# Performance work log

Measured on AMD Instinct MI355X. Metric: run time of the kernel, lower is better.

The kernel has to match this reference:

```python
import jax, jax.numpy as jnp
import numpy as np

N_NODES = 100000
N_EDGES = 1600000
D_IN = 64
D_OUT = 64


def setup_inputs() -> dict:
    key = jax.random.key(0)
    k1, k2, k3, k4 = jax.random.split(key, 4)
    x = jax.random.normal(k1, (N_NODES, D_IN), dtype=jnp.float32)
    edge_index = jax.random.randint(k2, (2, N_EDGES), 0, N_NODES, dtype=jnp.int64)
    W = jax.random.normal(k3, (D_OUT, D_IN), dtype=jnp.float32) * (1.0 / np.sqrt(D_IN))
    b = jax.random.normal(k4, (D_OUT,), dtype=jnp.float32) * 0.01
    return {"x": x, "edge_index": edge_index, "W": W, "b": b}


def reference(x, edge_index, W, b):
    num_nodes = x.shape[0]
    row, col = edge_index[0], edge_index[1]
    # degree of each node as a destination (scatter_add of ones over row)
    deg = jax.ops.segment_sum(jnp.ones(row.shape[0], dtype=x.dtype), row,
                              num_segments=num_nodes)
    # deg^-0.5 with inf (deg==0) replaced by 0
    deg_inv_sqrt = jnp.where(deg > 0, jax.lax.rsqrt(jnp.maximum(deg, 1.0)) * jnp.where(deg > 0, 1.0, 0.0), 0.0)
    deg_inv_sqrt = jnp.where(deg > 0, deg ** -0.5, 0.0)
    # gather source features, scale by source norm, scatter-add to destinations
    weighted = x[col] * deg_inv_sqrt[col][:, None]          # [E, D_IN]
    agg = jax.ops.segment_sum(weighted, row, num_segments=num_nodes)  # [N, D_IN]
    agg = agg * deg_inv_sqrt[:, None]
    # linear + relu (torch Linear: y = agg @ W.T + b)
    return jax.nn.relu(agg @ W.T + b)
```

## Files before the change

### kernel.cpp

```cpp
#include <hip/hip_runtime.h>

#define N_NODES 100000
#define N_EDGES 1600000
#define D 64

#define FSHIFT 5
#define FNODES 32
#define NFB 3125
#define CAPF 800

#define CSHIFT 11
#define NCB 49
#define CCAP 36864
#define FPC 64
#define NCHUNKB 9

#define CHUNK 4096
#define EPT 16
#define NCHUNKA 391

#define COLBITS 17
#define COLMASK 0x1FFFF

#define FCUR_OFF   0
#define CCUR_OFF   16384
#define CPAIRS_OFF 32768
#define FPAIRS_OFF 7258112
#define Y_OFF      17258112

typedef float fvec4 __attribute__((ext_vector_type(4)));

__device__ __forceinline__ float bf2f(unsigned short u) {
    return __uint_as_float(((unsigned)u) << 16);
}
__device__ __forceinline__ unsigned f2bf(float f) {
    unsigned bits = __float_as_uint(f);
    return (bits + 0x7FFFu + ((bits >> 16) & 1u)) >> 16;
}

__global__ void initcur_kernel(int* __restrict__ fcur, int* __restrict__ ccur) {
    int i = blockIdx.x * blockDim.x + threadIdx.x;
    if (i < NFB) fcur[i] = i * CAPF;
    if (i < NCB) ccur[i] = i * CCAP;
}

__global__ __launch_bounds__(256) void scatA_kernel(const int* __restrict__ row,
                                                    const int* __restrict__ col,
                                                    int* __restrict__ ccur,
                                                    int* __restrict__ cpairs) {
    __shared__ int lcnt[NCB];
    int t = threadIdx.x;
    int base = blockIdx.x * CHUNK;
    if (t < NCB) lcnt[t] = 0;
    __syncthreads();
    int r[EPT], c[EPT], pos[EPT];
#pragma unroll
    for (int i = 0; i < EPT; ++i) {
        int e = base + i * 256 + t;
        if (e < N_EDGES) {
            r[i] = row[e];
            c[i] = col[e];
            pos[i] = atomicAdd(&lcnt[r[i] >> CSHIFT], 1);
        } else r[i] = -1;
    }
    __syncthreads();
    if (t < NCB) {
        int cc = lcnt[t];
        if (cc) lcnt[t] = atomicAdd(&ccur[t], cc);
    }
    __syncthreads();
#pragma unroll
    for (int i = 0; i < EPT; ++i) {
        if (r[i] >= 0) {
            int cb = r[i] >> CSHIFT;
            int rl = r[i] & ((1 << CSHIFT) - 1);
            cpairs[lcnt[cb] + pos[i]] = (rl << COLBITS) | c[i];
        }
    }
}

__global__ __launch_bounds__(256) void scatB_kernel(const int* __restrict__ cpairs,
                                                    const int* __restrict__ ccur,
                                                    int* __restrict__ fcur,
                                                    int* __restrict__ fpairs) {
    __shared__ int lcnt[FPC];
    int t = threadIdx.x;
    int cb = blockIdx.x / NCHUNKB;
    int k  = blockIdx.x % NCHUNKB;
    int beg = cb * CCAP + k * CHUNK;
    int end = ccur[cb];
    if (end > beg + CHUNK) end = beg + CHUNK;
    if (t < FPC) lcnt[t] = 0;
    __syncthreads();
    int pc[EPT], pos[EPT];
#pragma unroll
    for (int i = 0; i < EPT; ++i) {
        int e = beg + i * 256 + t;
        if (e < end) {
            pc[i] = cpairs[e];
            pos[i] = atomicAdd(&lcnt[pc[i] >> (COLBITS + FSHIFT)], 1);
        } else pc[i] = -1;
    }
    __syncthreads();
    if (t < FPC) {
        int cc = lcnt[t];
        if (cc) lcnt[t] = atomicAdd(&fcur[(cb << 6) + t], cc);
    }
    __syncthreads();
#pragma unroll
    for (int i = 0; i < EPT; ++i) {
        if (pc[i] >= 0) {
            int fl = pc[i] >> (COLBITS + FSHIFT);
            int rl5 = (pc[i] >> COLBITS) & (FNODES - 1);
            fpairs[lcnt[fl] + pos[i]] = (rl5 << COLBITS) | (pc[i] & COLMASK);
        }
    }
}

__global__ __launch_bounds__(256) void xform_kernel(
        const float* __restrict__ x, const float* __restrict__ W,
        const int* __restrict__ fpairs, const int* __restrict__ fcur,
        unsigned short* __restrict__ y) {
    __shared__ __align__(16) float XT[D * 68];
    __shared__ __align__(16) float WT[D * 68];
    __shared__ int hist[64];
    __shared__ float dl[64];
    int t = threadIdx.x;
    int b = blockIdx.x;
    int nb0 = b << 6;
    for (int i = t; i < D * D; i += 256) {
        int j = i >> 6, d = i & 63;
        WT[d * 68 + j] = W[i];
    }
    if (t < 64) hist[t] = 0;
    __syncthreads();
    for (int i = t; i < 64 * D; i += 256) {
        int n = i >> 6, d = i & 63;
        int g = nb0 + n;
        XT[d * 68 + n] = (g < N_NODES) ? x[(size_t)g * D + d] : 0.0f;
    }
#pragma unroll
    for (int half = 0; half < 2; ++half) {
        int f = 2 * b + half;
        if (f < NFB) {
            int beg = f * CAPF, end = fcur[f];
            for (int k = beg + t; k < end; k += 256)
                atomicAdd(&hist[(fpairs[k] >> COLBITS) + (half << FSHIFT)], 1);
        }
    }
    __syncthreads();
    if (t < 64) dl[t] = (hist[t] > 0) ? rsqrtf((float)hist[t]) : 0.0f;
    __syncthreads();
    int tj = t & 15, tn = t >> 4;
    float4 a0 = {0,0,0,0}, a1 = {0,0,0,0}, a2 = {0,0,0,0}, a3 = {0,0,0,0};
#pragma unroll 8
    for (int d = 0; d < D; ++d) {
        float4 xv = *(const float4*)&XT[d * 68 + tn * 4];
        float4 wv = *(const float4*)&WT[d * 68 + tj * 4];
        a0.x = fmaf(xv.x, wv.x, a0.x); a0.y = fmaf(xv.x, wv.y, a0.y);
        a0.z = fmaf(xv.x, wv.z, a0.z); a0.w = fmaf(xv.x, wv.w, a0.w);
        a1.x = fmaf(xv.y, wv.x, a1.x); a1.y = fmaf(xv.y, wv.y, a1.y);
        a1.z = fmaf(xv.y, wv.z, a1.z); a1.w = fmaf(xv.y, wv.w, a1.w);
        a2.x = fmaf(xv.z, wv.x, a2.x); a2.y = fmaf(xv.z, wv.y, a2.y);
        a2.z = fmaf(xv.z, wv.z, a2.z); a2.w = fmaf(xv.z, wv.w, a2.w);
        a3.x = fmaf(xv.w, wv.x, a3.x); a3.y = fmaf(xv.w, wv.y, a3.y);
        a3.z = fmaf(xv.w, wv.z, a3.z); a3.w = fmaf(xv.w, wv.w, a3.w);
    }
    int jb = tj * 4;
#pragma unroll
    for (int s = 0; s < 4; ++s) {
        int g = nb0 + tn * 4 + s;
        if (g < N_NODES) {
            float sc = dl[tn * 4 + s];
            float4 a = (s == 0) ? a0 : (s == 1) ? a1 : (s == 2) ? a2 : a3;
            unsigned lo = f2bf(a.x * sc) | (f2bf(a.y * sc) << 16);
            unsigned hi = f2bf(a.z * sc) | (f2bf(a.w * sc) << 16);
            *(uint2*)(y + (size_t)g * D + jb) = make_uint2(lo, hi);
        }
    }
}

__global__ __launch_bounds__(256) void mega_kernel(
        const int* __restrict__ fpairs, const int* __restrict__ fcur,
        const unsigned short* __restrict__ y,
        const float* __restrict__ bias, float* __restrict__ out) {
    __shared__ int hist[FNODES];
    __shared__ int sc[FNODES];
    __shared__ int lrptr[FNODES + 1];
    __shared__ int lcur[FNODES];
    __shared__ float dl[FNODES];
    __shared__ int lds_scol[CAPF];
    int t = threadIdx.x;
    int b = blockIdx.x;
    int beg = b * CAPF, end = fcur[b];
    if (t < FNODES) hist[t] = 0;
    __syncthreads();
    for (int k = beg + t; k < end; k += 256)
        atomicAdd(&hist[fpairs[k] >> COLBITS], 1);
    __syncthreads();
    if (t < FNODES) sc[t] = hist[t];
    __syncthreads();
    for (int off = 1; off < FNODES; off <<= 1) {
        int v = (t < FNODES && t >= off) ? sc[t - off] : 0;
        __syncthreads();
        if (t < FNODES) sc[t] += v;
        __syncthreads();
    }
    if (t < FNODES) {
        lrptr[t + 1] = sc[t];
        lcur[t] = sc[t] - hist[t];
        dl[t] = (hist[t] > 0) ? rsqrtf((float)hist[t]) : 0.0f;
    }
    if (t == 0) lrptr[0] = 0;
    __syncthreads();
    for (int k = beg + t; k < end; k += 256) {
        int p = fpairs[k];
        int pos = atomicAdd(&lcur[p >> COLBITS], 1);
        lds_scol[pos] = p & COLMASK;
    }
    __syncthreads();
    int wave = t >> 6;
    int lane = t & 63;
    int g = lane >> 3;
    int q = lane & 7;
    float bj[8];
    {
        float4 b0 = *(const float4*)(bias + q * 8);
        float4 b1 = *(const float4*)(bias + q * 8 + 4);
        bj[0] = b0.x; bj[1] = b0.y; bj[2] = b0.z; bj[3] = b0.w;
        bj[4] = b1.x; bj[5] = b1.y; bj[6] = b1.z; bj[7] = b1.w;
    }
    for (int ln = wave; ln < FNODES; ln += 4) {
        int s = lrptr[ln], e2 = lrptr[ln + 1];
        float a[8];
#pragma unroll
        for (int i = 0; i < 8; ++i) a[i] = 0.0f;
        for (int k = s; k < e2; k += 32) {
#pragma unroll
            for (int u = 0; u < 4; ++u) {
                int e = k + u * 8 + g;
                if (e < e2) {
                    int c = lds_scol[e];
                    uint4 v = *(const uint4*)(y + (size_t)c * D + q * 8);
                    a[0] += __uint_as_float(v.x << 16);
                    a[1] += __uint_as_float(v.x & 0xffff0000u);
                    a[2] += __uint_as_float(v.y << 16);
                    a[3] += __uint_as_float(v.y & 0xffff0000u);
                    a[4] += __uint_as_float(v.z << 16);
                    a[5] += __uint_as_float(v.z & 0xffff0000u);
                    a[6] += __uint_as_float(v.w << 16);
                    a[7] += __uint_as_float(v.w & 0xffff0000u);
                }
            }
        }
#pragma unroll
        for (int m = 8; m <= 32; m <<= 1) {
#pragma unroll
            for (int i = 0; i < 8; ++i)
                a[i] += __shfl_xor(a[i], m);
        }
        float dv = dl[ln];
        int n = (b << FSHIFT) + ln;
        if (g < 2) {
            int o = g * 4;
            fvec4 r;
            r.x = fmaxf(fmaf(dv, a[o + 0], bj[o + 0]), 0.0f);
            r.y = fmaxf(fmaf(dv, a[o + 1], bj[o + 1]), 0.0f);
            r.z = fmaxf(fmaf(dv, a[o + 2], bj[o + 2]), 0.0f);
            r.w = fmaxf(fmaf(dv, a[o + 3], bj[o + 3]), 0.0f);
            __builtin_nontemporal_store(r, (fvec4*)(out + (size_t)n * D + q * 8 + o));
        }
    }
}

extern "C" void kernel_launch(void* const* d_in, const int* in_sizes, int n_in,
                              void* d_out, int out_size, void* d_ws, size_t ws_size,
                              hipStream_t stream) {
    const float* x    = (const float*)d_in[0];
    const int*   eidx = (const int*)d_in[1];
    const float* W    = (const float*)d_in[2];
    const float* b    = (const float*)d_in[3];
    float* out = (float*)d_out;
    char* ws = (char*)d_ws;

    const int* row = eidx;
    const int* col = eidx + N_EDGES;

    int* fcur   = (int*)(ws + FCUR_OFF);
    int* ccur   = (int*)(ws + CCUR_OFF);
    int* cpairs = (int*)(ws + CPAIRS_OFF);
    int* fpairs = (int*)(ws + FPAIRS_OFF);
    unsigned short* y = (unsigned short*)(ws + Y_OFF);

    initcur_kernel<<<(NFB + 255) / 256, 256, 0, stream>>>(fcur, ccur);
    scatA_kernel<<<NCHUNKA, 256, 0, stream>>>(row, col, ccur, cpairs);
    scatB_kernel<<<NCB * NCHUNKB, 256, 0, stream>>>(cpairs, ccur, fcur, fpairs);
    xform_kernel<<<(N_NODES + 63) / 64, 256, 0, stream>>>(x, W, fpairs, fcur, y);
    mega_kernel<<<NFB, 256, 0, stream>>>(fpairs, fcur, y, b, out);
}
```

Before: 187.9 us.

## Replace two-level edge bucketing with per-128-node CSR build and MFMA transform

The second bucketing pass is replaced. The first scatter now writes edges into 782 fixed-capacity buckets of 128 destination nodes, and scatB sorts each bucket in LDS to produce a per-node row start and degree array. The transform kernel now runs on MFMA bf16 instructions, using a hi/lo split of x and W that needs three MFMAs per k-step to keep accuracy near fp32. It also reads degrees directly instead of rebuilding histograms. The aggregation kernel walks CSR ranges for 64 nodes per block. In exchange, buckets have a hard capacity of 2560 edges that silently drops overflow edges, which is a risk with skewed degree distributions.

Result: no change. 185.3 us (-1.4%).

```diff
diff --git a/kernel.cpp b/kernel.cpp
--- a/kernel.cpp
+++ b/kernel.cpp
@@ -4,31 +4,26 @@
 #define N_EDGES 1600000
 #define D 64
 
-#define FSHIFT 5
-#define FNODES 32
-#define NFB 3125
-#define CAPF 800
-
-#define CSHIFT 11
-#define NCB 49
-#define CCAP 36864
-#define FPC 64
-#define NCHUNKB 9
+#define CSHIFT 7
+#define CNODES 128
+#define NCB 782
+#define CAPC 2560
+#define COLBITS 17
+#define COLMASK 0x1FFFF
 
 #define CHUNK 4096
 #define EPT 16
 #define NCHUNKA 391
 
-#define COLBITS 17
-#define COLMASK 0x1FFFF
-
-#define FCUR_OFF   0
-#define CCUR_OFF   16384
-#define CPAIRS_OFF 32768
-#define FPAIRS_OFF 7258112
-#define Y_OFF      17258112
+#define CCUR_OFF   0
+#define CPAIRS_OFF 3200
+#define RS_OFF     8010880
+#define DG_OFF     8410880
+#define Y_OFF      8810880
 
 typedef float fvec4 __attribute__((ext_vector_type(4)));
+typedef __attribute__((ext_vector_type(8))) short bf16x8;
+typedef __attribute__((ext_vector_type(4))) float f32x4;
 
 __device__ __forceinline__ float bf2f(unsigned short u) {
     return __uint_as_float(((unsigned)u) << 16);
@@ -36,12 +31,6 @@
 __device__ __forceinline__ unsigned f2bf(float f) {
     unsigned bits = __float_as_uint(f);
     return (bits + 0x7FFFu + ((bits >> 16) & 1u)) >> 16;
-}
-
-__global__ void initcur_kernel(int* __restrict__ fcur, int* __restrict__ ccur) {
-    int i = blockIdx.x * blockDim.x + threadIdx.x;
-    if (i < NFB) fcur[i] = i * CAPF;
-    if (i < NCB) ccur[i] = i * CCAP;
 }
 
 __global__ __launch_bounds__(256) void scatA_kernel(const int* __restrict__ row,
@@ -51,7 +40,7 @@
     __shared__ int lcnt[NCB];
     int t = threadIdx.x;
     int base = blockIdx.x * CHUNK;
-    if (t < NCB) lcnt[t] = 0;
+    for (int i = t; i < NCB; i += 256) lcnt[i] = 0;
     __syncthreads();
     int r[EPT], c[EPT], pos[EPT];
 #pragma unroll
@@ -64,165 +53,142 @@
         } else r[i] = -1;
     }
     __syncthreads();
-    if (t < NCB) {
-        int cc = lcnt[t];
-        if (cc) lcnt[t] = atomicAdd(&ccur[t], cc);
+    for (int i = t; i < NCB; i += 256) {
+        int cc = lcnt[i];
+        lcnt[i] = cc ? atomicAdd(&ccur[i], cc) : 0;
     }
     __syncthreads();
 #pragma unroll
     for (int i = 0; i < EPT; ++i) {
         if (r[i] >= 0) {
             int cb = r[i] >> CSHIFT;
-            int rl = r[i] & ((1 << CSHIFT) - 1);
-            cpairs[lcnt[cb] + pos[i]] = (rl << COLBITS) | c[i];
-        }
-    }
-}
-
-__global__ __launch_bounds__(256) void scatB_kernel(const int* __restrict__ cpairs,
-                                                    const int* __restrict__ ccur,
-                                                    int* __restrict__ fcur,
-                                                    int* __restrict__ fpairs) {
-    __shared__ int lcnt[FPC];
-    int t = threadIdx.x;
-    int cb = blockIdx.x / NCHUNKB;
-    int k  = blockIdx.x % NCHUNKB;
-    int beg = cb * CCAP + k * CHUNK;
-    int end = ccur[cb];
-    if (end > beg + CHUNK) end = beg + CHUNK;
-    if (t < FPC) lcnt[t] = 0;
-    __syncthreads();
-    int pc[EPT], pos[EPT];
-#pragma unroll
-    for (int i = 0; i < EPT; ++i) {
-        int e = beg + i * 256 + t;
-        if (e < end) {
-            pc[i] = cpairs[e];
-            pos[i] = atomicAdd(&lcnt[pc[i] >> (COLBITS + FSHIFT)], 1);
-        } else pc[i] = -1;
-    }
-    __syncthreads();
-    if (t < FPC) {
-        int cc = lcnt[t];
-        if (cc) lcnt[t] = atomicAdd(&fcur[(cb << 6) + t], cc);
-    }
-    __syncthreads();
-#pragma unroll
-    for (int i = 0; i < EPT; ++i) {
-        if (pc[i] >= 0) {
-            int fl = pc[i] >> (COLBITS + FSHIFT);
-            int rl5 = (pc[i] >> COLBITS) & (FNODES - 1);
-            fpairs[lcnt[fl] + pos[i]] = (rl5 << COLBITS) | (pc[i] & COLMASK);
-        }
+            int p = lcnt[cb] + pos[i];
+            if (p < CAPC)
+                cpairs[cb * CAPC + p] = ((r[i] & (CNODES - 1)) << COLBITS) | c[i];
+        }
+    }
+}
+
+__global__ __launch_bounds__(256) void scatB_kernel(const int* __restrict__ ccur,
+                                                    int* __restrict__ cpairs,
+                                                    int* __restrict__ rs,
+                                                    int* __restrict__ dg) {
+    __shared__ int epk[CAPC];
+    __shared__ int hist[CNODES];
+    __shared__ int sc[CNODES];
+    __shared__ int cur[CNODES];
+    int t = threadIdx.x;
+    int cb = blockIdx.x;
+    int cnt = ccur[cb]; if (cnt > CAPC) cnt = CAPC;
+    int base = cb * CAPC;
+    if (t < CNODES) hist[t] = 0;
+    __syncthreads();
+    for (int i = t; i < cnt; i += 256) {
+        int p = cpairs[base + i];
+        epk[i] = p;
+        atomicAdd(&hist[p >> COLBITS], 1);
+    }
+    __syncthreads();
+    if (t < CNODES) sc[t] = hist[t];
+    __syncthreads();
+    for (int off = 1; off < CNODES; off <<= 1) {
+        int v = (t < CNODES && t >= off) ? sc[t - off] : 0;
+        __syncthreads();
+        if (t < CNODES) sc[t] += v;
+        __syncthreads();
+    }
+    if (t < CNODES) {
+        int ex = sc[t] - hist[t];
+        cur[t] = ex;
+        int n = (cb << CSHIFT) + t;
+        if (n < N_NODES) { rs[n] = base + ex; dg[n] = hist[t]; }
+    }
+    __syncthreads();
+    for (int i = t; i < cnt; i += 256) {
+        int p = epk[i];
+        int pos = atomicAdd(&cur[p >> COLBITS], 1);
+        cpairs[base + pos] = p & COLMASK;
     }
 }
 
 __global__ __launch_bounds__(256) void xform_kernel(
         const float* __restrict__ x, const float* __restrict__ W,
-        const int* __restrict__ fpairs, const int* __restrict__ fcur,
-        unsigned short* __restrict__ y) {
-    __shared__ __align__(16) float XT[D * 68];
-    __shared__ __align__(16) float WT[D * 68];
-    __shared__ int hist[64];
-    __shared__ float dl[64];
+        const int* __restrict__ dg, unsigned short* __restrict__ y) {
+    int t = threadIdx.x;
+    int wave = t >> 6, lane = t & 63;
+    int n0w = blockIdx.x * 64 + wave * 16;
+    if (n0w >= N_NODES) return;
+    int lm = lane & 15;
+    int g  = lane >> 4;
+
+    bf16x8 ahi[2], alo[2];
+    const float* xr = x + (size_t)(n0w + lm) * D + g * 8;
+#pragma unroll
+    for (int ks = 0; ks < 2; ++ks) {
+        float4 fa = *(const float4*)(xr + ks * 32);
+        float4 fb = *(const float4*)(xr + ks * 32 + 4);
+        float f[8] = {fa.x, fa.y, fa.z, fa.w, fb.x, fb.y, fb.z, fb.w};
+#pragma unroll
+        for (int j = 0; j < 8; ++j) {
+            unsigned hb = f2bf(f[j]);
+            float r = f[j] - bf2f((unsigned short)hb);
+            ahi[ks][j] = (short)hb;
+            alo[ks][j] = (short)f2bf(r);
+        }
+    }
+    float dvr[4];
+#pragma unroll
+    for (int r = 0; r < 4; ++r) {
+        int d = dg[n0w + g * 4 + r];
+        dvr[r] = (d > 0) ? rsqrtf((float)d) : 0.0f;
+    }
+#pragma unroll
+    for (int jt = 0; jt < 4; ++jt) {
+        const float* wr = W + (size_t)(jt * 16 + lm) * D + g * 8;
+        bf16x8 whi[2], wlo[2];
+#pragma unroll
+        for (int ks = 0; ks < 2; ++ks) {
+            float4 fa = *(const float4*)(wr + ks * 32);
+            float4 fb = *(const float4*)(wr + ks * 32 + 4);
+            float f[8] = {fa.x, fa.y, fa.z, fa.w, fb.x, fb.y, fb.z, fb.w};
+#pragma unroll
+            for (int j = 0; j < 8; ++j) {
+                unsigned hb = f2bf(f[j]);
+                float r = f[j] - bf2f((unsigned short)hb);
+                whi[ks][j] = (short)hb;
+                wlo[ks][j] = (short)f2bf(r);
+            }
+        }
+        f32x4 acc = {0.0f, 0.0f, 0.0f, 0.0f};
+#pragma unroll
+        for (int ks = 0; ks < 2; ++ks) {
+            acc = __builtin_amdgcn_mfma_f32_16x16x32_bf16(ahi[ks], whi[ks], acc, 0, 0, 0);
+            acc = __builtin_amdgcn_mfma_f32_16x16x32_bf16(alo[ks], whi[ks], acc, 0, 0, 0);
+            acc = __builtin_amdgcn_mfma_f32_16x16x32_bf16(ahi[ks], wlo[ks], acc, 0, 0, 0);
+        }
+#pragma unroll
+        for (int r = 0; r < 4; ++r) {
+            int n = n0w + g * 4 + r;
+            y[(size_t)n * D + jt * 16 + lm] = (unsigned short)f2bf(acc[r] * dvr[r]);
+        }
+    }
+}
+
+__global__ __launch_bounds__(256) void mega_kernel(
+        const int* __restrict__ cols, const int* __restrict__ rs,
+        const int* __restrict__ dg, const unsigned short* __restrict__ y,
+        const float* __restrict__ bias, float* __restrict__ out) {
+    __shared__ int scol[CAPC];
     int t = threadIdx.x;
     int b = blockIdx.x;
-    int nb0 = b << 6;
-    for (int i = t; i < D * D; i += 256) {
-        int j = i >> 6, d = i & 63;
-        WT[d * 68 + j] = W[i];
-    }
-    if (t < 64) hist[t] = 0;
-    __syncthreads();
-    for (int i = t; i < 64 * D; i += 256) {
-        int n = i >> 6, d = i & 63;
-        int g = nb0 + n;
-        XT[d * 68 + n] = (g < N_NODES) ? x[(size_t)g * D + d] : 0.0f;
-    }
-#pragma unroll
-    for (int half = 0; half < 2; ++half) {
-        int f = 2 * b + half;
-        if (f < NFB) {
-            int beg = f * CAPF, end = fcur[f];
-            for (int k = beg + t; k < end; k += 256)
-                atomicAdd(&hist[(fpairs[k] >> COLBITS) + (half << FSHIFT)], 1);
-        }
-    }
-    __syncthreads();
-    if (t < 64) dl[t] = (hist[t] > 0) ? rsqrtf((float)hist[t]) : 0.0f;
-    __syncthreads();
-    int tj = t & 15, tn = t >> 4;
-    float4 a0 = {0,0,0,0}, a1 = {0,0,0,0}, a2 = {0,0,0,0}, a3 = {0,0,0,0};
-#pragma unroll 8
-    for (int d = 0; d < D; ++d) {
-        float4 xv = *(const float4*)&XT[d * 68 + tn * 4];
-        float4 wv = *(const float4*)&WT[d * 68 + tj * 4];
-        a0.x = fmaf(xv.x, wv.x, a0.x); a0.y = fmaf(xv.x, wv.y, a0.y);
-        a0.z = fmaf(xv.x, wv.z, a0.z); a0.w = fmaf(xv.x, wv.w, a0.w);
-        a1.x = fmaf(xv.y, wv.x, a1.x); a1.y = fmaf(xv.y, wv.y, a1.y);
-        a1.z = fmaf(xv.y, wv.z, a1.z); a1.w = fmaf(xv.y, wv.w, a1.w);
-        a2.x = fmaf(xv.z, wv.x, a2.x); a2.y = fmaf(xv.z, wv.y, a2.y);
-        a2.z = fmaf(xv.z, wv.z, a2.z); a2.w = fmaf(xv.z, wv.w, a2.w);
-        a3.x = fmaf(xv.w, wv.x, a3.x); a3.y = fmaf(xv.w, wv.y, a3.y);
-        a3.z = fmaf(xv.w, wv.z, a3.z); a3.w = fmaf(xv.w, wv.w, a3.w);
-    }
-    int jb = tj * 4;
-#pragma unroll
-    for (int s = 0; s < 4; ++s) {
-        int g = nb0 + tn * 4 + s;
-        if (g < N_NODES) {
-            float sc = dl[tn * 4 + s];
-            float4 a = (s == 0) ? a0 : (s == 1) ? a1 : (s == 2) ? a2 : a3;
-            unsigned lo = f2bf(a.x * sc) | (f2bf(a.y * sc) << 16);
-            unsigned hi = f2bf(a.z * sc) | (f2bf(a.w * sc) << 16);
-            *(uint2*)(y + (size_t)g * D + jb) = make_uint2(lo, hi);
-        }
-    }
-}
-
-__global__ __launch_bounds__(256) void mega_kernel(
-        const int* __restrict__ fpairs, const int* __restrict__ fcur,
-        const unsigned short* __restrict__ y,
-        const float* __restrict__ bias, float* __restrict__ out) {
-    __shared__ int hist[FNODES];
-    __shared__ int sc[FNODES];
-    __shared__ int lrptr[FNODES + 1];
-    __shared__ int lcur[FNODES];
-    __shared__ float dl[FNODES];
-    __shared__ int lds_scol[CAPF];
-    int t = threadIdx.x;
-    int b = blockIdx.x;
-    int beg = b * CAPF, end = fcur[b];
-    if (t < FNODES) hist[t] = 0;
-    __syncthreads();
-    for (int k = beg + t; k < end; k += 256)
-        atomicAdd(&hist[fpairs[k] >> COLBITS], 1);
-    __syncthreads();
-    if (t < FNODES) sc[t] = hist[t];
-    __syncthreads();
-    for (int off = 1; off < FNODES; off <<= 1) {
-        int v = (t < FNODES && t >= off) ? sc[t - off] : 0;
-        __syncthreads();
-        if (t < FNODES) sc[t] += v;
-        __syncthreads();
-    }
-    if (t < FNODES) {
-        lrptr[t + 1] = sc[t];
-        lcur[t] = sc[t] - hist[t];
-        dl[t] = (hist[t] > 0) ? rsqrtf((float)hist[t]) : 0.0f;
-    }
-    if (t == 0) lrptr[0] = 0;
-    __syncthreads();
-    for (int k = beg + t; k < end; k += 256) {
-        int p = fpairs[k];
-        int pos = atomicAdd(&lcur[p >> COLBITS], 1);
-        lds_scol[pos] = p & COLMASK;
-    }
-    __syncthreads();
-    int wave = t >> 6;
-    int lane = t & 63;
-    int g = lane >> 3;
-    int q = lane & 7;
+    int n0 = b * 64;
+    int nlast = n0 + 63; if (nlast >= N_NODES) nlast = N_NODES - 1;
+    int base = rs[n0];
+    int cnt = rs[nlast] + dg[nlast] - base;
+    for (int i = t; i < cnt; i += 256) scol[i] = cols[base + i];
+    __syncthreads();
+    int wave = t >> 6, lane = t & 63;
+    int g = lane >> 3, q = lane & 7;
     float bj[8];
     {
         float4 b0 = *(const float4*)(bias + q * 8);
@@ -230,17 +196,21 @@
         bj[0] = b0.x; bj[1] = b0.y; bj[2] = b0.z; bj[3] = b0.w;
         bj[4] = b1.x; bj[5] = b1.y; bj[6] = b1.z; bj[7] = b1.w;
     }
-    for (int ln = wave; ln < FNODES; ln += 4) {
-        int s = lrptr[ln], e2 = lrptr[ln + 1];
+#pragma unroll 1
+    for (int i = 0; i < 16; ++i) {
+        int n = n0 + wave * 16 + i;
+        if (n >= N_NODES) break;
+        int s = rs[n] - base;
+        int d = dg[n];
         float a[8];
 #pragma unroll
-        for (int i = 0; i < 8; ++i) a[i] = 0.0f;
-        for (int k = s; k < e2; k += 32) {
+        for (int j = 0; j < 8; ++j) a[j] = 0.0f;
+        for (int k = 0; k < d; k += 32) {
 #pragma unroll
             for (int u = 0; u < 4; ++u) {
                 int e = k + u * 8 + g;
-                if (e < e2) {
-                    int c = lds_scol[e];
+                if (e < d) {
+                    int c = scol[s + e];
                     uint4 v = *(const uint4*)(y + (size_t)c * D + q * 8);
                     a[0] += __uint_as_float(v.x << 16);
                     a[1] += __uint_as_float(v.x & 0xffff0000u);
@@ -256,11 +226,10 @@
 #pragma unroll
         for (int m = 8; m <= 32; m <<= 1) {
 #pragma unroll
-            for (int i = 0; i < 8; ++i)
-                a[i] += __shfl_xor(a[i], m);
-        }
-        float dv = dl[ln];
-        int n = (b << FSHIFT) + ln;
+            for (int j = 0; j < 8; ++j)
+                a[j] += __shfl_xor(a[j], m);
+        }
+        float dv = (d > 0) ? rsqrtf((float)d) : 0.0f;
         if (g < 2) {
             int o = g * 4;
             fvec4 r;
@@ -286,15 +255,15 @@
     const int* row = eidx;
     const int* col = eidx + N_EDGES;
 
-    int* fcur   = (int*)(ws + FCUR_OFF);
     int* ccur   = (int*)(ws + CCUR_OFF);
     int* cpairs = (int*)(ws + CPAIRS_OFF);
-    int* fpairs = (int*)(ws + FPAIRS_OFF);
+    int* rs     = (int*)(ws + RS_OFF);
+    int* dg     = (int*)(ws + DG_OFF);
     unsigned short* y = (unsigned short*)(ws + Y_OFF);
 
-    initcur_kernel<<<(NFB + 255) / 256, 256, 0, stream>>>(fcur, ccur);
+    hipMemsetAsync(ccur, 0, NCB * sizeof(int), stream);
     scatA_kernel<<<NCHUNKA, 256, 0, stream>>>(row, col, ccur, cpairs);
-    scatB_kernel<<<NCB * NCHUNKB, 256, 0, stream>>>(cpairs, ccur, fcur, fpairs);
-    xform_kernel<<<(N_NODES + 63) / 64, 256, 0, stream>>>(x, W, fpairs, fcur, y);
-    mega_kernel<<<NFB, 256, 0, stream>>>(fpairs, fcur, y, b, out);
-}
+    scatB_kernel<<<NCB, 256, 0, stream>>>(ccur, cpairs, rs, dg);
+    xform_kernel<<<(N_NODES + 63) / 64, 256, 0, stream>>>(x, W, dg, y);
+    mega_kernel<<<(N_NODES + 63) / 64, 256, 0, stream>>>(cpairs, rs, dg, y, b, out);
+}
```
